# Optimization experiments

Measured on AMD Instinct MI355X. Metric: run time of the kernel, lower is better.

## Reference

```python
import jax, jax.numpy as jnp
import numpy as np

N_NODES = 50000
N_EDGES = 1600000
IN_CH = 128
OUT_CH = 64
N_HEADS = 4


def setup_inputs() -> dict:
    key = jax.random.key(0)
    k1, k2, k3, k4, k5 = jax.random.split(key, 5)
    x_source = jax.random.normal(k1, (N_NODES, IN_CH), dtype=jnp.float32)
    edge_tgt = jax.random.randint(k2, (N_EDGES,), 0, N_NODES, dtype=jnp.int32)
    edge_src = jax.random.randint(k3, (N_EDGES,), 0, N_NODES, dtype=jnp.int32)
    edge_vals = jnp.ones((N_EDGES,), dtype=jnp.float32)
    # per-head learned params (xavier_uniform-ish scale)
    w_scale = float(np.sqrt(6.0 / (IN_CH + OUT_CH)))
    weight = jax.random.uniform(k4, (N_HEADS, IN_CH, OUT_CH), dtype=jnp.float32,
                                minval=-w_scale, maxval=w_scale)
    a_scale = float(np.sqrt(6.0 / (2 * OUT_CH)))
    att_weight = jax.random.uniform(k5, (N_HEADS, 2 * OUT_CH), dtype=jnp.float32,
                                    minval=-a_scale, maxval=a_scale)
    return {"x_source": x_source, "edge_tgt": edge_tgt, "edge_src": edge_src,
            "edge_vals": edge_vals, "weight": weight, "att_weight": att_weight}


def _can_forward(x_source, edge_tgt, edge_src, edge_vals, weight, att_weight):
    n_nodes = x_source.shape[0]
    out_ch = weight.shape[-1]
    # per-head linear transform: [N, H, O]
    x_msg = jnp.einsum('ni,hio->nho', x_source, weight)
    # gather per-edge source/target messages: [E, H, O]
    src_msg = x_msg[edge_src]
    tgt_msg = x_msg[edge_tgt]
    # attention score = cat([src, tgt]) @ att_weight, split halves: [E, H]
    aw_s = att_weight[:, :out_ch]
    aw_t = att_weight[:, out_ch:]
    e = jnp.einsum('eho,ho->eh', src_msg, aw_s) + jnp.einsum('eho,ho->eh', tgt_msg, aw_t)
    e = jax.nn.leaky_relu(e, negative_slope=0.01)  # default torch slope
    e = e * edge_vals[:, None]  # multiply by neighborhood values pre-softmax
    # sparse softmax over each target row (dim=1 of the sparse matrix)
    row_max = jax.ops.segment_max(e, edge_tgt, num_segments=n_nodes)  # [N, H]
    e_exp = jnp.exp(e - row_max[edge_tgt])
    row_sum = jax.ops.segment_sum(e_exp, edge_tgt, num_segments=n_nodes)  # [N, H]
    alpha = e_exp / row_sum[edge_tgt]  # [E, H]
    # weighted aggregate of source messages per target node: [N, H, O]
    out = jax.ops.segment_sum(alpha[:, :, None] * src_msg, edge_tgt,
                              num_segments=n_nodes)
    # concat heads -> [N, H*O]
    return out.reshape(n_nodes, -1)


def reference(x_source, edge_tgt, edge_src, edge_vals, weight, att_weight):
    return _can_forward(x_source, edge_tgt, edge_src, edge_vals, weight, att_weight)
```

## Files before the change

kernel.cpp:

```cpp
#include <hip/hip_runtime.h>
#include <hip/hip_bf16.h>
#include <hip/hip_fp16.h>
#include <math.h>

#define N_NODES 50000
#define N_EDGES 1600000
#define IN_CH   128
#define OUT_CH  64
#define N_HEADS 4
#define CH      (N_HEADS * OUT_CH)

#define NPB   64
#define BINS  782
#define CAPB  3072
#define CHUNK 4000

typedef __attribute__((ext_vector_type(8))) _Float16 f16x8;
typedef __attribute__((ext_vector_type(4))) float f32x4;

__device__ __forceinline__ __half2 u2h2(unsigned u) {
  union { unsigned u; __half2 h; } c; c.u = u; return c.h;
}

__global__ __launch_bounds__(256) void prep_kernel(
    const float* __restrict__ w, unsigned short* __restrict__ wb2,
    int* __restrict__ gcur)
{
  if (blockIdx.x < 128) {
    int i = blockIdx.x * 256 + threadIdx.x;
    int j = i & 7, lane = (i >> 3) & 63, kc = (i >> 9) & 3, mb = i >> 11;
    int k = kc * 32 + (lane >> 4) * 8 + j;
    int ch = mb * 16 + (lane & 15);
    int h = ch >> 6, o = ch & 63;
    wb2[i] = __half_as_ushort(__float2half_rn(w[(h * IN_CH + k) * OUT_CH + o]));
  } else {
    for (int b = threadIdx.x; b < BINS; b += 256) gcur[b] = b * CAPB;
  }
}

__global__ __launch_bounds__(256) void gemm_mfma(
    const float* __restrict__ x, const unsigned short* __restrict__ wb2,
    const float* __restrict__ aw,
    unsigned short* __restrict__ xmsg, float* __restrict__ sbuf, float* __restrict__ tbuf)
{
  const int lane = threadIdx.x & 63;
  const int wv   = threadIdx.x >> 6;
  const int q    = lane >> 4;
  const int l16  = lane & 15;
  const int nb   = blockIdx.x * 128 + wv * 32;

  f16x8 bfrag[2][4];
  #pragma unroll
  for (int t = 0; t < 2; ++t) {
    int node = min(nb + t * 16 + l16, N_NODES - 1);
    const float* xp = x + (size_t)node * IN_CH + q * 8;
    #pragma unroll
    for (int kc = 0; kc < 4; ++kc) {
      f32x4 lo = *(const f32x4*)(xp + kc * 32);
      f32x4 hi = *(const f32x4*)(xp + kc * 32 + 4);
      f16x8 b;
      b[0] = (_Float16)lo[0]; b[1] = (_Float16)lo[1];
      b[2] = (_Float16)lo[2]; b[3] = (_Float16)lo[3];
      b[4] = (_Float16)hi[0]; b[5] = (_Float16)hi[1];
      b[6] = (_Float16)hi[2]; b[7] = (_Float16)hi[3];
      bfrag[t][kc] = b;
    }
  }

  f32x4 acc[2][16];
  #pragma unroll
  for (int t = 0; t < 2; ++t)
    #pragma unroll
    for (int mb = 0; mb < 16; ++mb)
      acc[t][mb] = (f32x4){0.f, 0.f, 0.f, 0.f};

  #pragma unroll
  for (int kc = 0; kc < 4; ++kc) {
    #pragma unroll
    for (int mb = 0; mb < 16; ++mb) {
      f16x8 a = *(const f16x8*)(wb2 + ((size_t)(mb * 4 + kc) * 64 + lane) * 8);
      acc[0][mb] = __builtin_amdgcn_mfma_f32_16x16x32_f16(a, bfrag[0][kc], acc[0][mb], 0, 0, 0);
      acc[1][mb] = __builtin_amdgcn_mfma_f32_16x16x32_f16(a, bfrag[1][kc], acc[1][mb], 0, 0, 0);
    }
  }

  #pragma unroll
  for (int t = 0; t < 2; ++t) {
    const int node = nb + t * 16 + l16;
    const bool valid = node < N_NODES;

    float sv[4] = {0.f, 0.f, 0.f, 0.f};
    float tv[4] = {0.f, 0.f, 0.f, 0.f};
    #pragma unroll
    for (int mb = 0; mb < 16; ++mb) {
      ushort4 pk;
      pk.x = __half_as_ushort(__float2half_rn(acc[t][mb][0]));
      pk.y = __half_as_ushort(__float2half_rn(acc[t][mb][1]));
      pk.z = __half_as_ushort(__float2half_rn(acc[t][mb][2]));
      pk.w = __half_as_ushort(__float2half_rn(acc[t][mb][3]));
      if (valid)
        *(ushort4*)(xmsg + (size_t)node * CH + mb * 16 + q * 4) = pk;

      const int h = mb >> 2;
      const int o = (mb & 3) * 16 + q * 4;
      #pragma unroll
      for (int reg = 0; reg < 4; ++reg) {
        float as_ = aw[h * 128 + o + reg];
        float at_ = aw[h * 128 + 64 + o + reg];
        sv[h] += acc[t][mb][reg] * as_;
        tv[h] += acc[t][mb][reg] * at_;
      }
    }
    #pragma unroll
    for (int hh = 0; hh < 4; ++hh) {
      sv[hh] += __shfl_xor(sv[hh], 16); sv[hh] += __shfl_xor(sv[hh], 32);
      tv[hh] += __shfl_xor(tv[hh], 16); tv[hh] += __shfl_xor(tv[hh], 32);
    }
    float svq = (q == 0) ? sv[0] : (q == 1) ? sv[1] : (q == 2) ? sv[2] : sv[3];
    float tvq = (q == 0) ? tv[0] : (q == 1) ? tv[1] : (q == 2) ? tv[2] : tv[3];
    if (valid) {
      sbuf[node * 4 + q] = svq;
      tbuf[node * 4 + q] = tvq;
    }
  }
}

__global__ __launch_bounds__(256) void bin_scatter(
    const int* __restrict__ etgt, const int* __restrict__ esrc,
    const float* __restrict__ eval, int* __restrict__ gcur, int2* __restrict__ binned)
{
  __shared__ int lhist[BINS];
  __shared__ int lbase[BINS];
  __shared__ unsigned short stg[CHUNK];

  const int tid = threadIdx.x;
  const int e0 = blockIdx.x * CHUNK;
  const int n = min(CHUNK, N_EDGES - e0);

  for (int b = tid; b < BINS; b += 256) lhist[b] = 0;
  __syncthreads();

  for (int i = tid; i < n; i += 256) {
    int t = etgt[e0 + i];
    stg[i] = (unsigned short)t;
    atomicAdd(&lhist[t >> 6], 1);
  }
  __syncthreads();

  for (int b = tid; b < BINS; b += 256) {
    int c = lhist[b];
    lbase[b] = c ? atomicAdd(&gcur[b], c) : 0;
    lhist[b] = 0;
  }
  __syncthreads();

  for (int i = tid; i < n; i += 256) {
    int t = (int)stg[i];
    int b = t >> 6;
    int r = atomicAdd(&lhist[b], 1);
    int pos = lbase[b] + r;
    if (pos < (b + 1) * CAPB) {
      int pack = esrc[e0 + i] | ((t & 63) << 16);
      binned[pos] = make_int2(pack, __float_as_int(eval[e0 + i]));
    }
  }
}

__global__ __launch_bounds__(256) void build_csr(
    const int* __restrict__ gcur, const int2* __restrict__ binned,
    int2* __restrict__ csr, int* __restrict__ deg, int* __restrict__ rowstart)
{
  __shared__ int nh[NPB];
  __shared__ int npre[NPB];
  __shared__ __align__(16) int2 stg[CAPB];

  const int tid = threadIdx.x;
  const int b = blockIdx.x;
  const int base = b * CAPB;
  const int cnt = min(gcur[b] - base, CAPB);

  if (tid < NPB) nh[tid] = 0;
  __syncthreads();

  for (int i = tid; i < cnt; i += 256) {
    int2 e = binned[base + i];
    stg[i] = e;
    atomicAdd(&nh[(e.x >> 16) & 63], 1);
  }
  __syncthreads();

  if (tid < 64) {
    int v = nh[tid];
    int sc = v;
    #pragma unroll
    for (int off = 1; off < 64; off <<= 1) {
      int u = __shfl_up(sc, off);
      if (tid >= off) sc += u;
    }
    npre[tid] = sc - v;
    int node = b * NPB + tid;
    if (node < N_NODES) { deg[node] = v; rowstart[node] = base + sc - v; }
    nh[tid] = 0;
  }
  __syncthreads();

  for (int i = tid; i < cnt; i += 256) {
    int2 e = stg[i];
    int tl = (e.x >> 16) & 63;
    int r = atomicAdd(&nh[tl], 1);
    csr[base + npre[tl] + r] = e;
  }
}

__global__ __launch_bounds__(256) void aggregate_kernel(
    const int* __restrict__ deg, const int* __restrict__ rowstart,
    const int2* __restrict__ csr,
    const float* __restrict__ sbuf, const float* __restrict__ tbuf,
    const unsigned short* __restrict__ xmsg, float* __restrict__ out)
{
  const int lane = threadIdx.x & 63;
  const int wave = threadIdx.x >> 6;
  const int n = blockIdx.x * 4 + wave;
  if (n >= N_NODES) return;

  __shared__ __align__(16) float p_lds[4][64][4];
  __shared__ int s_lds[4][64];

  const int d = deg[n];
  const int rs0 = rowstart[n];
  const int seg  = lane & 31;
  const int half = lane >> 5;
  const int hh4  = seg >> 3;

  float4 tn4 = *(const float4*)(tbuf + (size_t)n * 4);
  float tn[4] = {tn4.x, tn4.y, tn4.z, tn4.w};

  float m[4]    = {-INFINITY, -INFINITY, -INFINITY, -INFINITY};
  float psum[4] = {0.f, 0.f, 0.f, 0.f};
  __half2 hacc[4];
  #pragma unroll
  for (int j = 0; j < 4; ++j) hacc[j] = __float2half2_rn(0.f);

  for (int base = 0; base < d; base += 64) {
    const int cnt = min(64, d - base);
    const bool act = lane < cnt;

    float sc[4] = {-INFINITY, -INFINITY, -INFINITY, -INFINITY};
    int s = 0;
    if (act) {
      int2 ev = csr[(size_t)rs0 + base + lane];
      s = ev.x & 0xffff;
      float v = __int_as_float(ev.y);
      float4 sv4 = *(const float4*)(sbuf + (size_t)s * 4);
      float svv[4] = {sv4.x, sv4.y, sv4.z, sv4.w};
      #pragma unroll
      for (int hh = 0; hh < 4; ++hh) {
        float t = svv[hh] + tn[hh];
        t = (t > 0.f) ? t : 0.01f * t;
        sc[hh] = t * v;
      }
    }

    float bm[4] = {sc[0], sc[1], sc[2], sc[3]};
    #pragma unroll
    for (int hh = 0; hh < 4; ++hh)
      #pragma unroll
      for (int off = 32; off; off >>= 1)
        bm[hh] = fmaxf(bm[hh], __shfl_xor(bm[hh], off));

    float p[4];
    #pragma unroll
    for (int hh = 0; hh < 4; ++hh) {
      float nm = fmaxf(m[hh], bm[hh]);
      float r = (m[hh] == -INFINITY) ? 0.f : __expf(m[hh] - nm);
      psum[hh] *= r;
      if (hh == hh4) {
        __half2 rh = __float2half2_rn(r);
        #pragma unroll
        for (int j = 0; j < 4; ++j) hacc[j] = __hmul2(hacc[j], rh);
      }
      m[hh] = nm;
      p[hh] = act ? __expf(sc[hh] - nm) : 0.f;
      psum[hh] += p[hh];
    }

    if (act) {
      s_lds[wave][lane] = s;
      *(float4*)(&p_lds[wave][lane][0]) = make_float4(p[0], p[1], p[2], p[3]);
    }
    __builtin_amdgcn_wave_barrier();

    int k = 0;
    for (; k + 8 <= cnt; k += 8) {
      int sA = s_lds[wave][k + 0 + half];
      int sB = s_lds[wave][k + 2 + half];
      int sC = s_lds[wave][k + 4 + half];
      int sD = s_lds[wave][k + 6 + half];
      uint4 rA = *(const uint4*)(xmsg + (size_t)sA * CH + seg * 8);
      uint4 rB = *(const uint4*)(xmsg + (size_t)sB * CH + seg * 8);
      uint4 rC = *(const uint4*)(xmsg + (size_t)sC * CH + seg * 8);
      uint4 rD = *(const uint4*)(xmsg + (size_t)sD * CH + seg * 8);
      __half2 qA = __float2half2_rn(p_lds[wave][k + 0 + half][hh4]);
      __half2 qB = __float2half2_rn(p_lds[wave][k + 2 + half][hh4]);
      __half2 qC = __float2half2_rn(p_lds[wave][k + 4 + half][hh4]);
      __half2 qD = __float2half2_rn(p_lds[wave][k + 6 + half][hh4]);
      hacc[0] = __hfma2(qA, u2h2(rA.x), hacc[0]);
      hacc[1] = __hfma2(qA, u2h2(rA.y), hacc[1]);
      hacc[2] = __hfma2(qA, u2h2(rA.z), hacc[2]);
      hacc[3] = __hfma2(qA, u2h2(rA.w), hacc[3]);
      hacc[0] = __hfma2(qB, u2h2(rB.x), hacc[0]);
      hacc[1] = __hfma2(qB, u2h2(rB.y), hacc[1]);
      hacc[2] = __hfma2(qB, u2h2(rB.z), hacc[2]);
      hacc[3] = __hfma2(qB, u2h2(rB.w), hacc[3]);
      hacc[0] = __hfma2(qC, u2h2(rC.x), hacc[0]);
      hacc[1] = __hfma2(qC, u2h2(rC.y), hacc[1]);
      hacc[2] = __hfma2(qC, u2h2(rC.z), hacc[2]);
      hacc[3] = __hfma2(qC, u2h2(rC.w), hacc[3]);
      hacc[0] = __hfma2(qD, u2h2(rD.x), hacc[0]);
      hacc[1] = __hfma2(qD, u2h2(rD.y), hacc[1]);
      hacc[2] = __hfma2(qD, u2h2(rD.z), hacc[2]);
      hacc[3] = __hfma2(qD, u2h2(rD.w), hacc[3]);
    }
    for (; k < cnt; k += 2) {
      int e = k + half;
      if (e < cnt) {
        int sA = s_lds[wave][e];
        uint4 rA = *(const uint4*)(xmsg + (size_t)sA * CH + seg * 8);
        __half2 qA = __float2half2_rn(p_lds[wave][e][hh4]);
        hacc[0] = __hfma2(qA, u2h2(rA.x), hacc[0]);
        hacc[1] = __hfma2(qA, u2h2(rA.y), hacc[1]);
        hacc[2] = __hfma2(qA, u2h2(rA.z), hacc[2]);
        hacc[3] = __hfma2(qA, u2h2(rA.w), hacc[3]);
      }
    }
    __builtin_amdgcn_wave_barrier();
  }

  float acc[8];
  #pragma unroll
  for (int j = 0; j < 4; ++j) {
    acc[2*j]   = __low2float(hacc[j]);
    acc[2*j+1] = __high2float(hacc[j]);
  }
  #pragma unroll
  for (int j = 0; j < 8; ++j) acc[j] += __shfl_xor(acc[j], 32);
  #pragma unroll
  for (int hh = 0; hh < 4; ++hh)
    #pragma unroll
    for (int off = 32; off; off >>= 1)
      psum[hh] += __shfl_xor(psum[hh], off);

  float rs = psum[hh4];
  float inv = (rs > 0.f) ? 1.0f / rs : 0.f;
  const int o = half * 4;
  float4 o4 = make_float4(acc[o+0]*inv, acc[o+1]*inv, acc[o+2]*inv, acc[o+3]*inv);
  *(float4*)(out + (size_t)n * CH + seg * 8 + o) = o4;
}

extern "C" void kernel_launch(void* const* d_in, const int* in_sizes, int n_in,
                              void* d_out, int out_size, void* d_ws, size_t ws_size,
                              hipStream_t stream) {
  const float* x    = (const float*)d_in[0];
  const int*   etgt = (const int*)  d_in[1];
  const int*   esrc = (const int*)  d_in[2];
  const float* evl  = (const float*)d_in[3];
  const float* w    = (const float*)d_in[4];
  const float* aw   = (const float*)d_in[5];
  float* out = (float*)d_out;

  char* ws = (char*)d_ws;
  unsigned short* wb2  = (unsigned short*)(ws);
  unsigned short* xmsg = (unsigned short*)(ws + 65536);
  float* sbuf     = (float*)(ws + 25665536);
  float* tbuf     = (float*)(ws + 26465536);
  int*   gcur     = (int*)  (ws + 27265536);
  int*   deg      = (int*)  (ws + 27269632);
  int*   rowstart = (int*)  (ws + 27470336);
  int2*  binned   = (int2*) (ws + 27671040);
  int2*  csr      = (int2*) (ws + 46889472);

  prep_kernel<<<129, 256, 0, stream>>>(w, wb2, gcur);
  gemm_mfma<<<(N_NODES + 127) / 128, 256, 0, stream>>>(x, wb2, aw, xmsg, sbuf, tbuf);
  bin_scatter<<<(N_EDGES + CHUNK - 1) / CHUNK, 256, 0, stream>>>(etgt, esrc, evl, gcur, binned);
  build_csr<<<BINS, 256, 0, stream>>>(gcur, binned, csr, deg, rowstart);
  aggregate_kernel<<<(N_NODES + 3) / 4, 256, 0, stream>>>(deg, rowstart, csr,
                                                          sbuf, tbuf, xmsg, out);
}
```

Baseline: 291.8 us.

## Fuse CSR build into aggregation kernel with per-bin LDS sorting

Removes the separate build_csr and aggregate kernels and replaces them with one kernel per 32-node bin. That kernel counting-sorts the bin's edges into LDS, then aggregates each node's neighbours straight from LDS. Bins shrink from 64 to 32 nodes and per-bin capacity drops to 1280, so the sorted edge list fits in shared memory. This avoids a kernel launch and the global write and re-read of the CSR, deg and rowstart arrays. In exchange there are far fewer blocks, each wave processes 8 nodes in sequence, and a smaller capacity margin per bin.

```diff
diff --git a/kernel.cpp b/kernel.cpp
--- a/kernel.cpp
+++ b/kernel.cpp
@@ -10,9 +10,9 @@
 #define N_HEADS 4
 #define CH      (N_HEADS * OUT_CH)
 
-#define NPB   64
-#define BINS  782
-#define CAPB  3072
+#define NPB   32
+#define BINS  1563
+#define CAPB  1280
 #define CHUNK 4000
 
 typedef __attribute__((ext_vector_type(8))) _Float16 f16x8;
@@ -143,7 +143,7 @@
   for (int i = tid; i < n; i += 256) {
     int t = etgt[e0 + i];
     stg[i] = (unsigned short)t;
-    atomicAdd(&lhist[t >> 6], 1);
+    atomicAdd(&lhist[t >> 5], 1);
   }
   __syncthreads();
 
@@ -156,23 +156,25 @@
 
   for (int i = tid; i < n; i += 256) {
     int t = (int)stg[i];
-    int b = t >> 6;
+    int b = t >> 5;
     int r = atomicAdd(&lhist[b], 1);
     int pos = lbase[b] + r;
     if (pos < (b + 1) * CAPB) {
-      int pack = esrc[e0 + i] | ((t & 63) << 16);
+      int pack = esrc[e0 + i] | ((t & 31) << 16);
       binned[pos] = make_int2(pack, __float_as_int(eval[e0 + i]));
     }
   }
 }
 
-__global__ __launch_bounds__(256) void build_csr(
+__global__ __launch_bounds__(256) void aggregate_fused(
     const int* __restrict__ gcur, const int2* __restrict__ binned,
-    int2* __restrict__ csr, int* __restrict__ deg, int* __restrict__ rowstart)
+    const float* __restrict__ sbuf, const float* __restrict__ tbuf,
+    const unsigned short* __restrict__ xmsg, float* __restrict__ out)
 {
+  __shared__ __align__(16) int2 s2[CAPB];
   __shared__ int nh[NPB];
   __shared__ int npre[NPB];
-  __shared__ __align__(16) int2 stg[CAPB];
+  __shared__ __align__(16) float p_lds[4][64][4];
 
   const int tid = threadIdx.x;
   const int b = blockIdx.x;
@@ -182,179 +184,166 @@
   if (tid < NPB) nh[tid] = 0;
   __syncthreads();
 
+  for (int i = tid; i < cnt; i += 256)
+    atomicAdd(&nh[(binned[base + i].x >> 16) & 31], 1);
+  __syncthreads();
+
+  if (tid < NPB) {
+    int v = nh[tid];
+    int sc = v;
+    #pragma unroll
+    for (int off = 1; off < NPB; off <<= 1) {
+      int u = __shfl_up(sc, off);
+      if (tid >= off) sc += u;
+    }
+    npre[tid] = sc - v;
+    nh[tid] = 0;
+  }
+  __syncthreads();
+
   for (int i = tid; i < cnt; i += 256) {
     int2 e = binned[base + i];
-    stg[i] = e;
-    atomicAdd(&nh[(e.x >> 16) & 63], 1);
-  }
-  __syncthreads();
-
-  if (tid < 64) {
-    int v = nh[tid];
-    int sc = v;
-    #pragma unroll
-    for (int off = 1; off < 64; off <<= 1) {
-      int u = __shfl_up(sc, off);
-      if (tid >= off) sc += u;
-    }
-    npre[tid] = sc - v;
-    int node = b * NPB + tid;
-    if (node < N_NODES) { deg[node] = v; rowstart[node] = base + sc - v; }
-    nh[tid] = 0;
-  }
-  __syncthreads();
-
-  for (int i = tid; i < cnt; i += 256) {
-    int2 e = stg[i];
-    int tl = (e.x >> 16) & 63;
+    int tl = (e.x >> 16) & 31;
     int r = atomicAdd(&nh[tl], 1);
-    csr[base + npre[tl] + r] = e;
-  }
-}
-
-__global__ __launch_bounds__(256) void aggregate_kernel(
-    const int* __restrict__ deg, const int* __restrict__ rowstart,
-    const int2* __restrict__ csr,
-    const float* __restrict__ sbuf, const float* __restrict__ tbuf,
-    const unsigned short* __restrict__ xmsg, float* __restrict__ out)
-{
-  const int lane = threadIdx.x & 63;
-  const int wave = threadIdx.x >> 6;
-  const int n = blockIdx.x * 4 + wave;
-  if (n >= N_NODES) return;
-
-  __shared__ __align__(16) float p_lds[4][64][4];
-  __shared__ int s_lds[4][64];
-
-  const int d = deg[n];
-  const int rs0 = rowstart[n];
+    s2[npre[tl] + r] = e;
+  }
+  __syncthreads();
+
+  const int lane = tid & 63;
+  const int wave = tid >> 6;
   const int seg  = lane & 31;
   const int half = lane >> 5;
   const int hh4  = seg >> 3;
 
-  float4 tn4 = *(const float4*)(tbuf + (size_t)n * 4);
-  float tn[4] = {tn4.x, tn4.y, tn4.z, tn4.w};
-
-  float m[4]    = {-INFINITY, -INFINITY, -INFINITY, -INFINITY};
-  float psum[4] = {0.f, 0.f, 0.f, 0.f};
-  __half2 hacc[4];
-  #pragma unroll
-  for (int j = 0; j < 4; ++j) hacc[j] = __float2half2_rn(0.f);
-
-  for (int base = 0; base < d; base += 64) {
-    const int cnt = min(64, d - base);
-    const bool act = lane < cnt;
-
-    float sc[4] = {-INFINITY, -INFINITY, -INFINITY, -INFINITY};
-    int s = 0;
-    if (act) {
-      int2 ev = csr[(size_t)rs0 + base + lane];
-      s = ev.x & 0xffff;
-      float v = __int_as_float(ev.y);
-      float4 sv4 = *(const float4*)(sbuf + (size_t)s * 4);
-      float svv[4] = {sv4.x, sv4.y, sv4.z, sv4.w};
+  for (int nn = 0; nn < 8; ++nn) {
+    const int tl = wave * 8 + nn;
+    const int n = b * NPB + tl;
+    if (n >= N_NODES) break;
+
+    const int d = nh[tl];
+    const int rs0 = npre[tl];
+
+    float4 tn4 = *(const float4*)(tbuf + (size_t)n * 4);
+    float tn[4] = {tn4.x, tn4.y, tn4.z, tn4.w};
+
+    float m[4]    = {-INFINITY, -INFINITY, -INFINITY, -INFINITY};
+    float psum[4] = {0.f, 0.f, 0.f, 0.f};
+    __half2 hacc[4];
+    #pragma unroll
+    for (int j = 0; j < 4; ++j) hacc[j] = __float2half2_rn(0.f);
+
+    for (int bb = 0; bb < d; bb += 64) {
+      const int cnt2 = min(64, d - bb);
+      const bool act = lane < cnt2;
+
+      float sc[4] = {-INFINITY, -INFINITY, -INFINITY, -INFINITY};
+      if (act) {
+        int2 ev = s2[rs0 + bb + lane];
+        int s = ev.x & 0xffff;
+        float v = __int_as_float(ev.y);
+        float4 sv4 = *(const float4*)(sbuf + (size_t)s * 4);
+        float svv[4] = {sv4.x, sv4.y, sv4.z, sv4.w};
+        #pragma unroll
+        for (int hh = 0; hh < 4; ++hh) {
+          float t = svv[hh] + tn[hh];
+          t = (t > 0.f) ? t : 0.01f * t;
+          sc[hh] = t * v;
+        }
+      }
+
+      float bm[4] = {sc[0], sc[1], sc[2], sc[3]};
+      #pragma unroll
+      for (int hh = 0; hh < 4; ++hh)
+        #pragma unroll
+        for (int off = 32; off; off >>= 1)
+          bm[hh] = fmaxf(bm[hh], __shfl_xor(bm[hh], off));
+
+      float p[4];
       #pragma unroll
       for (int hh = 0; hh < 4; ++hh) {
-        float t = svv[hh] + tn[hh];
-        t = (t > 0.f) ? t : 0.01f * t;
-        sc[hh] = t * v;
-      }
-    }
-
-    float bm[4] = {sc[0], sc[1], sc[2], sc[3]};
-    #pragma unroll
-    for (int hh = 0; hh < 4; ++hh)
-      #pragma unroll
-      for (int off = 32; off; off >>= 1)
-        bm[hh] = fmaxf(bm[hh], __shfl_xor(bm[hh], off));
-
-    float p[4];
-    #pragma unroll
-    for (int hh = 0; hh < 4; ++hh) {
-      float nm = fmaxf(m[hh], bm[hh]);
-      float r = (m[hh] == -INFINITY) ? 0.f : __expf(m[hh] - nm);
-      psum[hh] *= r;
-      if (hh == hh4) {
-        __half2 rh = __float2half2_rn(r);
-        #pragma unroll
-        for (int j = 0; j < 4; ++j) hacc[j] = __hmul2(hacc[j], rh);
-      }
-      m[hh] = nm;
-      p[hh] = act ? __expf(sc[hh] - nm) : 0.f;
-      psum[hh] += p[hh];
-    }
-
-    if (act) {
-      s_lds[wave][lane] = s;
-      *(float4*)(&p_lds[wave][lane][0]) = make_float4(p[0], p[1], p[2], p[3]);
-    }
-    __builtin_amdgcn_wave_barrier();
-
-    int k = 0;
-    for (; k + 8 <= cnt; k += 8) {
-      int sA = s_lds[wave][k + 0 + half];
-      int sB = s_lds[wave][k + 2 + half];
-      int sC = s_lds[wave][k + 4 + half];
-      int sD = s_lds[wave][k + 6 + half];
-      uint4 rA = *(const uint4*)(xmsg + (size_t)sA * CH + seg * 8);
-      uint4 rB = *(const uint4*)(xmsg + (size_t)sB * CH + seg * 8);
-      uint4 rC = *(const uint4*)(xmsg + (size_t)sC * CH + seg * 8);
-      uint4 rD = *(const uint4*)(xmsg + (size_t)sD * CH + seg * 8);
-      __half2 qA = __float2half2_rn(p_lds[wave][k + 0 + half][hh4]);
-      __half2 qB = __float2half2_rn(p_lds[wave][k + 2 + half][hh4]);
-      __half2 qC = __float2half2_rn(p_lds[wave][k + 4 + half][hh4]);
-      __half2 qD = __float2half2_rn(p_lds[wave][k + 6 + half][hh4]);
-      hacc[0] = __hfma2(qA, u2h2(rA.x), hacc[0]);
-      hacc[1] = __hfma2(qA, u2h2(rA.y), hacc[1]);
-      hacc[2] = __hfma2(qA, u2h2(rA.z), hacc[2]);
-      hacc[3] = __hfma2(qA, u2h2(rA.w), hacc[3]);
-      hacc[0] = __hfma2(qB, u2h2(rB.x), hacc[0]);
-      hacc[1] = __hfma2(qB, u2h2(rB.y), hacc[1]);
-      hacc[2] = __hfma2(qB, u2h2(rB.z), hacc[2]);
-      hacc[3] = __hfma2(qB, u2h2(rB.w), hacc[3]);
-      hacc[0] = __hfma2(qC, u2h2(rC.x), hacc[0]);
-      hacc[1] = __hfma2(qC, u2h2(rC.y), hacc[1]);
-      hacc[2] = __hfma2(qC, u2h2(rC.z), hacc[2]);
-      hacc[3] = __hfma2(qC, u2h2(rC.w), hacc[3]);
-      hacc[0] = __hfma2(qD, u2h2(rD.x), hacc[0]);
-      hacc[1] = __hfma2(qD, u2h2(rD.y), hacc[1]);
-      hacc[2] = __hfma2(qD, u2h2(rD.z), hacc[2]);
-      hacc[3] = __hfma2(qD, u2h2(rD.w), hacc[3]);
-    }
-    for (; k < cnt; k += 2) {
-      int e = k + half;
-      if (e < cnt) {
-        int sA = s_lds[wave][e];
+        float nm = fmaxf(m[hh], bm[hh]);
+        float r = (m[hh] == -INFINITY) ? 0.f : __expf(m[hh] - nm);
+        psum[hh] *= r;
+        if (hh == hh4) {
+          __half2 rh = __float2half2_rn(r);
+          #pragma unroll
+          for (int j = 0; j < 4; ++j) hacc[j] = __hmul2(hacc[j], rh);
+        }
+        m[hh] = nm;
+        p[hh] = act ? __expf(sc[hh] - nm) : 0.f;
+        psum[hh] += p[hh];
+      }
+
+      if (act)
+        *(float4*)(&p_lds[wave][lane][0]) = make_float4(p[0], p[1], p[2], p[3]);
+      __builtin_amdgcn_wave_barrier();
+
+      int k = 0;
+      for (; k + 8 <= cnt2; k += 8) {
+        int sA = s2[rs0 + bb + k + 0 + half].x & 0xffff;
+        int sB = s2[rs0 + bb + k + 2 + half].x & 0xffff;
+        int sC = s2[rs0 + bb + k + 4 + half].x & 0xffff;
+        int sD = s2[rs0 + bb + k + 6 + half].x & 0xffff;
         uint4 rA = *(const uint4*)(xmsg + (size_t)sA * CH + seg * 8);
-        __half2 qA = __float2half2_rn(p_lds[wave][e][hh4]);
+        uint4 rB = *(const uint4*)(xmsg + (size_t)sB * CH + seg * 8);
+        uint4 rC = *(const uint4*)(xmsg + (size_t)sC * CH + seg * 8);
+        uint4 rD = *(const uint4*)(xmsg + (size_t)sD * CH + seg * 8);
+        __half2 qA = __float2half2_rn(p_lds[wave][k + 0 + half][hh4]);
+        __half2 qB = __float2half2_rn(p_lds[wave][k + 2 + half][hh4]);
+        __half2 qC = __float2half2_rn(p_lds[wave][k + 4 + half][hh4]);
+        __half2 qD = __float2half2_rn(p_lds[wave][k + 6 + half][hh4]);
         hacc[0] = __hfma2(qA, u2h2(rA.x), hacc[0]);
         hacc[1] = __hfma2(qA, u2h2(rA.y), hacc[1]);
         hacc[2] = __hfma2(qA, u2h2(rA.z), hacc[2]);
         hacc[3] = __hfma2(qA, u2h2(rA.w), hacc[3]);
-      }
-    }
-    __builtin_amdgcn_wave_barrier();
-  }
-
-  float acc[8];
-  #pragma unroll
-  for (int j = 0; j < 4; ++j) {
-    acc[2*j]   = __low2float(hacc[j]);
-    acc[2*j+1] = __high2float(hacc[j]);
-  }
-  #pragma unroll
-  for (int j = 0; j < 8; ++j) acc[j] += __shfl_xor(acc[j], 32);
-  #pragma unroll
-  for (int hh = 0; hh < 4; ++hh)
-    #pragma unroll
-    for (int off = 32; off; off >>= 1)
-      psum[hh] += __shfl_xor(psum[hh], off);
-
-  float rs = psum[hh4];
-  float inv = (rs > 0.f) ? 1.0f / rs : 0.f;
-  const int o = half * 4;
-  float4 o4 = make_float4(acc[o+0]*inv, acc[o+1]*inv, acc[o+2]*inv, acc[o+3]*inv);
-  *(float4*)(out + (size_t)n * CH + seg * 8 + o) = o4;
+        hacc[0] = __hfma2(qB, u2h2(rB.x), hacc[0]);
+        hacc[1] = __hfma2(qB, u2h2(rB.y), hacc[1]);
+        hacc[2] = __hfma2(qB, u2h2(rB.z), hacc[2]);
+        hacc[3] = __hfma2(qB, u2h2(rB.w), hacc[3]);
+        hacc[0] = __hfma2(qC, u2h2(rC.x), hacc[0]);
+        hacc[1] = __hfma2(qC, u2h2(rC.y), hacc[1]);
+        hacc[2] = __hfma2(qC, u2h2(rC.z), hacc[2]);
+        hacc[3] = __hfma2(qC, u2h2(rC.w), hacc[3]);
+        hacc[0] = __hfma2(qD, u2h2(rD.x), hacc[0]);
+        hacc[1] = __hfma2(qD, u2h2(rD.y), hacc[1]);
+        hacc[2] = __hfma2(qD, u2h2(rD.z), hacc[2]);
+        hacc[3] = __hfma2(qD, u2h2(rD.w), hacc[3]);
+      }
+      for (; k < cnt2; k += 2) {
+        int e = k + half;
+        if (e < cnt2) {
+          int sA = s2[rs0 + bb + e].x & 0xffff;
+          uint4 rA = *(const uint4*)(xmsg + (size_t)sA * CH + seg * 8);
+          __half2 qA = __float2half2_rn(p_lds[wave][e][hh4]);
+          hacc[0] = __hfma2(qA, u2h2(rA.x), hacc[0]);
+          hacc[1] = __hfma2(qA, u2h2(rA.y), hacc[1]);
+          hacc[2] = __hfma2(qA, u2h2(rA.z), hacc[2]);
+          hacc[3] = __hfma2(qA, u2h2(rA.w), hacc[3]);
+        }
+      }
+      __builtin_amdgcn_wave_barrier();
+    }
+
+    float acc[8];
+    #pragma unroll
+    for (int j = 0; j < 4; ++j) {
+      acc[2*j]   = __low2float(hacc[j]);
+      acc[2*j+1] = __high2float(hacc[j]);
+    }
+    #pragma unroll
+    for (int j = 0; j < 8; ++j) acc[j] += __shfl_xor(acc[j], 32);
+    #pragma unroll
+    for (int hh = 0; hh < 4; ++hh)
+      #pragma unroll
+      for (int off = 32; off; off >>= 1)
+        psum[hh] += __shfl_xor(psum[hh], off);
+
+    float rs = psum[hh4];
+    float inv = (rs > 0.f) ? 1.0f / rs : 0.f;
+    const int o = half * 4;
+    float4 o4 = make_float4(acc[o+0]*inv, acc[o+1]*inv, acc[o+2]*inv, acc[o+3]*inv);
+    *(float4*)(out + (size_t)n * CH + seg * 8 + o) = o4;
+  }
 }
 
 extern "C" void kernel_launch(void* const* d_in, const int* in_sizes, int n_in,
@@ -374,15 +363,10 @@
   float* sbuf     = (float*)(ws + 25665536);
   float* tbuf     = (float*)(ws + 26465536);
   int*   gcur     = (int*)  (ws + 27265536);
-  int*   deg      = (int*)  (ws + 27269632);
-  int*   rowstart = (int*)  (ws + 27470336);
-  int2*  binned   = (int2*) (ws + 27671040);
-  int2*  csr      = (int2*) (ws + 46889472);
+  int2*  binned   = (int2*) (ws + 27273728);
 
   prep_kernel<<<129, 256, 0, stream>>>(w, wb2, gcur);
   gemm_mfma<<<(N_NODES + 127) / 128, 256, 0, stream>>>(x, wb2, aw, xmsg, sbuf, tbuf);
   bin_scatter<<<(N_EDGES + CHUNK - 1) / CHUNK, 256, 0, stream>>>(etgt, esrc, evl, gcur, binned);
-  build_csr<<<BINS, 256, 0, stream>>>(gcur, binned, csr, deg, rowstart);
-  aggregate_kernel<<<(N_NODES + 3) / 4, 256, 0, stream>>>(deg, rowstart, csr,
-                                                          sbuf, tbuf, xmsg, out);
-}
+  aggregate_fused<<<BINS, 256, 0, stream>>>(gcur, binned, sbuf, tbuf, xmsg, out);
+}
```

Result: no change. 291.6 us (-0.1%).
